# Kernel tuning notes

Measured on AMD Instinct MI355X. Metric: run time of the kernel, lower is better.

Reference implementation:

```python
import jax, jax.numpy as jnp
import numpy as np

N_NODES = 50000
N_EDGES = 800000
G_DIM = 128
H1_DIM = 128
H2_DIM = 128
N_REL = 8          # 2 * n_speakers**2, n_speakers = 2
N_BASES = 30


def setup_inputs() -> dict:
    key = jax.random.key(0)
    ks = jax.random.split(key, 10)
    node_features = jax.random.normal(ks[0], (N_NODES, G_DIM), jnp.float32)
    edge_index = jax.random.randint(ks[1], (2, N_EDGES), 0, N_NODES, jnp.int32)
    edge_norm = jax.random.uniform(ks[2], (N_EDGES,), jnp.float32)
    edge_type = jax.random.randint(ks[3], (N_EDGES,), 0, N_REL, jnp.int32)
    # RGCN basis-decomposition params
    w_comp = jax.random.normal(ks[4], (N_REL, N_BASES), jnp.float32) / np.sqrt(N_BASES)
    bases = jax.random.normal(ks[5], (N_BASES, G_DIM, H1_DIM), jnp.float32) / np.sqrt(G_DIM)
    loop_weight = jax.random.normal(ks[6], (G_DIM, H1_DIM), jnp.float32) / np.sqrt(G_DIM)
    bias1 = jnp.zeros((H1_DIM,), jnp.float32)
    # GraphConv params
    W2 = jax.random.normal(ks[7], (H1_DIM, H2_DIM), jnp.float32) / np.sqrt(H1_DIM)
    bias2 = jnp.zeros((H2_DIM,), jnp.float32)
    return dict(node_features=node_features, edge_index=edge_index,
                edge_norm=edge_norm, edge_type=edge_type,
                w_comp=w_comp, bases=bases, loop_weight=loop_weight, bias1=bias1,
                W2=W2, bias2=bias2)


def reference(node_features, edge_index, edge_norm, edge_type,
              w_comp, bases, loop_weight, bias1, W2, bias2):
    N = node_features.shape[0]
    src, dst = edge_index[0], edge_index[1]

    # ---- RGCNConv (DGL RelGraphConv, basis regularizer, self_loop + bias) ----
    # relation weights from bases: [R, g, h1]
    weight = jnp.einsum('rb,bio->rio', w_comp, bases)
    # project all nodes by every relation (R is small), then gather per edge
    xw = jnp.einsum('ni,rio->rno', node_features, weight)   # [R, N, h1]
    msgs = xw[edge_type, src] * edge_norm[:, None]          # [E, h1]
    agg = jax.ops.segment_sum(msgs, dst, num_segments=N)    # scatter-add to dst
    h = agg + node_features @ loop_weight + bias1           # [N, h1]

    # ---- GraphConv (DGL, norm='both', edge_weight; degrees are UNweighted) ----
    ones = jnp.ones_like(edge_norm)
    out_deg = jax.ops.segment_sum(ones, src, num_segments=N)
    in_deg = jax.ops.segment_sum(ones, dst, num_segments=N)
    norm_src = jnp.clip(out_deg, 1.0) ** -0.5               # [N]
    norm_dst = jnp.clip(in_deg, 1.0) ** -0.5                # [N]
    m2 = (h * norm_src[:, None])[src] * edge_norm[:, None]  # [E, h1]
    agg2 = jax.ops.segment_sum(m2, dst, num_segments=N)     # [N, h1]
    out = (agg2 * norm_dst[:, None]) @ W2 + bias2           # [N, h2]
    return out
```

## Files before the change

kernel.cpp:

```cpp
#include <hip/hip_runtime.h>

#define NN 50000
#define EE 800000
#define NB 30
#define NJ 1152
#define NSB 49
#define NPART 16
#define RANGE 3136
#define NSLICE 64
#define ESL 12500
#define NPAD 50176

typedef __attribute__((ext_vector_type(8))) short short8;
typedef __attribute__((ext_vector_type(4))) float f32x4;

__device__ __forceinline__ unsigned short f2bf(float f) {
  unsigned u = __float_as_uint(f);
  u += 0x7FFF + ((u >> 16) & 1);
  return (unsigned short)(u >> 16);
}
__device__ __forceinline__ float bf2f(unsigned short s) {
  return __uint_as_float(((unsigned)s) << 16);
}

__global__ __launch_bounds__(256) void k_prep(const float* __restrict__ wcomp,
                                              const float* __restrict__ bases,
                                              const float* __restrict__ loopw,
                                              const float* __restrict__ W2,
                                              const float* __restrict__ X,
                                              unsigned short* __restrict__ Wt,
                                              unsigned short* __restrict__ W2t,
                                              unsigned short* __restrict__ Xbf) {
  int b = blockIdx.x;
  if (b < 576) {
    int idx = b * 256 + threadIdx.x;
    int j = idx >> 7, k = idx & 127;
    float v;
    if (j < 1024) {
      int r = j >> 7, o = j & 127;
      float s = 0.f;
#pragma unroll
      for (int bb = 0; bb < NB; ++bb)
        s = fmaf(wcomp[r * NB + bb], bases[((size_t)bb * 128 + k) * 128 + o], s);
      v = s;
    } else {
      v = loopw[k * 128 + (j - 1024)];
    }
    Wt[idx] = f2bf(v);
    if (idx < 128 * 128) W2t[idx] = f2bf(W2[k * 128 + j]);
  } else {
    int i = ((b - 576) * 256 + threadIdx.x) * 4;
    float4 v = *(const float4*)(X + i);
    uint2 o;
    o.x = (unsigned)f2bf(v.x) | ((unsigned)f2bf(v.y) << 16);
    o.y = (unsigned)f2bf(v.z) | ((unsigned)f2bf(v.w) << 16);
    *(uint2*)(Xbf + i) = o;
  }
}

__global__ __launch_bounds__(256) void k_hist(const int* __restrict__ EI,
                                              int* __restrict__ pdin, int* __restrict__ pdout) {
  __shared__ int hist[RANGE];
  int b = blockIdx.x;
  int kind = b & 1;
  int sl = (b >> 1) & (NSLICE - 1);
  int r = b >> 7;
  const int base = r * RANGE;
  const int* vals = kind ? EI : EI + EE;
  int* part = kind ? pdout : pdin;
  for (int j = threadIdx.x; j < RANGE; j += 256) hist[j] = 0;
  __syncthreads();
  const int e0 = sl * ESL;
  for (int i = threadIdx.x; i < ESL / 4; i += 256) {
    int4 d = *(const int4*)(vals + e0 + i * 4);
    int x;
    x = d.x - base; if ((unsigned)x < RANGE) atomicAdd(&hist[x], 1);
    x = d.y - base; if ((unsigned)x < RANGE) atomicAdd(&hist[x], 1);
    x = d.z - base; if ((unsigned)x < RANGE) atomicAdd(&hist[x], 1);
    x = d.w - base; if ((unsigned)x < RANGE) atomicAdd(&hist[x], 1);
  }
  __syncthreads();
  for (int j = threadIdx.x; j < RANGE; j += 256)
    part[sl * NPAD + base + j] = hist[j];
}

__global__ __launch_bounds__(256) void k_scan_a(const int* __restrict__ pdin,
                                                const int* __restrict__ pdout,
                                                int* __restrict__ din,
                                                int* __restrict__ dout,
                                                int* __restrict__ bsum) {
  __shared__ int wsum[4];
  int b = blockIdx.x, t = threadIdx.x;
  int lane = t & 63, w = t >> 6;
  int i0 = b * 1024 + t * 4;
  int4 acc = {0, 0, 0, 0}, od = {0, 0, 0, 0};
  for (int sl = 0; sl < NSLICE; ++sl) {
    int4 a = *(const int4*)(pdin + sl * NPAD + i0);
    int4 o = *(const int4*)(pdout + sl * NPAD + i0);
    acc.x += a.x; acc.y += a.y; acc.z += a.z; acc.w += a.w;
    od.x += o.x; od.y += o.y; od.z += o.z; od.w += o.w;
  }
  *(int4*)(din + i0) = acc;
  *(int4*)(dout + i0) = od;
  int sv = acc.x + acc.y + acc.z + acc.w;
#pragma unroll
  for (int off = 32; off; off >>= 1) sv += __shfl_down(sv, off, 64);
  if (lane == 0) wsum[w] = sv;
  __syncthreads();
  if (t == 0) bsum[b] = wsum[0] + wsum[1] + wsum[2] + wsum[3];
}

__global__ void k_scan_b(int* __restrict__ bsum, int* __restrict__ row_ptr) {
  int t = threadIdx.x;
  int v = (t < NSB) ? bsum[t] : 0;
  int orig = v;
#pragma unroll
  for (int off = 1; off < 64; off <<= 1) {
    int u = __shfl_up(v, off, 64);
    if (t >= off) v += u;
  }
  if (t < NSB) bsum[t] = v - orig;
  if (t == 0) row_ptr[NN] = EE;
}

__global__ __launch_bounds__(256) void k_scan_c(const int* __restrict__ din,
                                                const int* __restrict__ bsum,
                                                int* __restrict__ row_ptr,
                                                int* __restrict__ cursor) {
  __shared__ int wsum[4];
  int b = blockIdx.x, t = threadIdx.x;
  int lane = t & 63, w = t >> 6;
  int i0 = b * 1024 + t * 4;
  int4 d = *(const int4*)(din + i0);
  int sth = d.x + d.y + d.z + d.w;
  int v = sth;
#pragma unroll
  for (int off = 1; off < 64; off <<= 1) {
    int u = __shfl_up(v, off, 64);
    if (lane >= off) v += u;
  }
  if (lane == 63) wsum[w] = v;
  __syncthreads();
  int woff = 0;
  for (int j = 0; j < w; ++j) woff += wsum[j];
  int base = bsum[b] + woff + (v - sth);
  if (i0 + 0 <= NN) { row_ptr[i0 + 0] = base; if (i0 + 0 < NN) cursor[i0 + 0] = base; } base += d.x;
  if (i0 + 1 <= NN) { row_ptr[i0 + 1] = base; if (i0 + 1 < NN) cursor[i0 + 1] = base; } base += d.y;
  if (i0 + 2 <= NN) { row_ptr[i0 + 2] = base; if (i0 + 2 < NN) cursor[i0 + 2] = base; } base += d.z;
  if (i0 + 3 <= NN) { row_ptr[i0 + 3] = base; if (i0 + 3 < NN) cursor[i0 + 3] = base; }
}

__global__ void k_csr(const int* __restrict__ src, const int* __restrict__ dst,
                      const int* __restrict__ ety, const float* __restrict__ enorm,
                      int* __restrict__ cursor, int2* __restrict__ em1) {
  int e = blockIdx.x * 256 + threadIdx.x;
  if (e < EE) {
    int pos = atomicAdd(&cursor[dst[e]], 1);
    int s = src[e];
    int wb = __float_as_int(enorm[e]);
    em1[pos] = make_int2(s * NJ + ety[e] * 128, wb);
  }
}

__global__ __launch_bounds__(256) void k_gemm(const unsigned short* __restrict__ A,
                                              const unsigned short* __restrict__ B,
                                              unsigned short* __restrict__ Cbf,
                                              float* __restrict__ Cf,
                                              const float* __restrict__ bias,
                                              int M, int ldc) {
  __shared__ unsigned short As[128 * 136];
  __shared__ unsigned short Bs[128 * 136];
  const int m0 = blockIdx.x * 128, j0 = blockIdx.y * 128;
  const int t = threadIdx.x;
  for (int i = t; i < 2048; i += 256) {
    int r = i >> 4, c = i & 15;
    uint4 va = {0, 0, 0, 0};
    int gr = m0 + r;
    if (gr < M) va = *(const uint4*)(A + (size_t)gr * 128 + c * 8);
    *(uint4*)(&As[r * 136 + c * 8]) = va;
    uint4 vb = *(const uint4*)(B + (size_t)(j0 + r) * 128 + c * 8);
    *(uint4*)(&Bs[r * 136 + c * 8]) = vb;
  }
  __syncthreads();

  const int lane = t & 63, wave = t >> 6;
  const int wr = (wave >> 1) * 64, wc = (wave & 1) * 64;
  const int lr = lane & 15, lk = (lane >> 4) * 8;

  f32x4 acc[4][4];
#pragma unroll
  for (int m = 0; m < 4; ++m)
#pragma unroll
    for (int n = 0; n < 4; ++n) acc[m][n] = (f32x4){0.f, 0.f, 0.f, 0.f};

#pragma unroll
  for (int kt = 0; kt < 4; ++kt) {
    short8 af[4], bfr[4];
#pragma unroll
    for (int m = 0; m < 4; ++m)
      af[m] = *(const short8*)(&As[(wr + m * 16 + lr) * 136 + kt * 32 + lk]);
#pragma unroll
    for (int n = 0; n < 4; ++n)
      bfr[n] = *(const short8*)(&Bs[(wc + n * 16 + lr) * 136 + kt * 32 + lk]);
#pragma unroll
    for (int m = 0; m < 4; ++m)
#pragma unroll
      for (int n = 0; n < 4; ++n)
        acc[m][n] = __builtin_amdgcn_mfma_f32_16x16x32_bf16(af[m], bfr[n], acc[m][n], 0, 0, 0);
  }

#pragma unroll
  for (int m = 0; m < 4; ++m) {
    int rbase = m0 + wr + m * 16 + (lane >> 4) * 4;
#pragma unroll
    for (int i = 0; i < 4; ++i) {
      int row = rbase + i;
      if (row >= M) continue;
      if (Cbf) {
        unsigned short* cr = Cbf + (size_t)row * ldc + j0 + wc;
#pragma unroll
        for (int n = 0; n < 4; ++n) cr[n * 16 + lr] = f2bf(acc[m][n][i]);
      } else {
        float* cr = Cf + (size_t)row * ldc + j0 + wc;
#pragma unroll
        for (int n = 0; n < 4; ++n) cr[n * 16 + lr] = acc[m][n][i] + bias[j0 + wc + n * 16 + lr];
      }
    }
  }
}

#define UNR 8

__global__ __launch_bounds__(256) void k_agg1(const unsigned short* __restrict__ xw,
                                              const int2* __restrict__ em1,
                                              const int* __restrict__ row_ptr,
                                              const int* __restrict__ deg_out,
                                              const float* __restrict__ bias1,
                                              unsigned short* __restrict__ hs) {
  int gw = (blockIdx.x * blockDim.x + threadIdx.x) >> 6;
  int lane = threadIdx.x & 63;
  if (gw >= NN) return;
  int beg = row_ptr[gw], end = row_ptr[gw + 1];
  float a0 = 0.f, a1 = 0.f;
  for (int i = beg; i < end; i += UNR) {
    int2 md[UNR];
    unsigned v[UNR];
#pragma unroll
    for (int j = 0; j < UNR; ++j) {
      int idx = i + j;
      idx = idx < end ? idx : end - 1;
      md[j] = em1[idx];
      if (i + j >= end) md[j].y = 0;
    }
#pragma unroll
    for (int j = 0; j < UNR; ++j)
      v[j] = *(const unsigned*)(xw + (size_t)(unsigned)md[j].x + lane * 2);
#pragma unroll
    for (int j = 0; j < UNR; ++j) {
      float w = __int_as_float(md[j].y);
      a0 = fmaf(w, bf2f((unsigned short)(v[j] & 0xffff)), a0);
      a1 = fmaf(w, bf2f((unsigned short)(v[j] >> 16)), a1);
    }
  }
  unsigned vl = *(const unsigned*)(xw + (size_t)gw * NJ + 1024 + lane * 2);
  float ns = rsqrtf(fmaxf((float)deg_out[gw], 1.f));
  float h0 = (a0 + bf2f((unsigned short)(vl & 0xffff)) + bias1[lane * 2]) * ns;
  float h1 = (a1 + bf2f((unsigned short)(vl >> 16)) + bias1[lane * 2 + 1]) * ns;
  unsigned o = (unsigned)f2bf(h0) | ((unsigned)f2bf(h1) << 16);
  *(unsigned*)(hs + (size_t)gw * 128 + lane * 2) = o;
}

__global__ __launch_bounds__(256) void k_agg2(const unsigned short* __restrict__ hs,
                                              const int2* __restrict__ em1,
                                              const int* __restrict__ row_ptr,
                                              unsigned short* __restrict__ zb) {
  int gw = (blockIdx.x * blockDim.x + threadIdx.x) >> 6;
  int lane = threadIdx.x & 63;
  if (gw >= NN) return;
  int beg = row_ptr[gw], end = row_ptr[gw + 1];
  float a0 = 0.f, a1 = 0.f;
  for (int i = beg; i < end; i += UNR) {
    int2 md[UNR];
    unsigned v[UNR];
#pragma unroll
    for (int j = 0; j < UNR; ++j) {
      int idx = i + j;
      idx = idx < end ? idx : end - 1;
      md[j] = em1[idx];
      if (i + j >= end) md[j].y = 0;
    }
#pragma unroll
    for (int j = 0; j < UNR; ++j) {
      unsigned srcn = (((unsigned)md[j].x) >> 7) / 9u;
      v[j] = *(const unsigned*)(hs + ((size_t)srcn << 7) + lane * 2);
    }
#pragma unroll
    for (int j = 0; j < UNR; ++j) {
      float w = __int_as_float(md[j].y);
      a0 = fmaf(w, bf2f((unsigned short)(v[j] & 0xffff)), a0);
      a1 = fmaf(w, bf2f((unsigned short)(v[j] >> 16)), a1);
    }
  }
  float nd = rsqrtf(fmaxf((float)(end - beg), 1.f));
  unsigned o = (unsigned)f2bf(a0 * nd) | ((unsigned)f2bf(a1 * nd) << 16);
  *(unsigned*)(zb + (size_t)gw * 128 + lane * 2) = o;
}

extern "C" void kernel_launch(void* const* d_in, const int* in_sizes, int n_in,
                              void* d_out, int out_size, void* d_ws, size_t ws_size,
                              hipStream_t stream) {
  const float* X = (const float*)d_in[0];
  const int* EI = (const int*)d_in[1];
  const float* enorm = (const float*)d_in[2];
  const int* etype = (const int*)d_in[3];
  const float* wcomp = (const float*)d_in[4];
  const float* bases = (const float*)d_in[5];
  const float* loopw = (const float*)d_in[6];
  const float* bias1 = (const float*)d_in[7];
  const float* W2 = (const float*)d_in[8];
  const float* bias2 = (const float*)d_in[9];
  float* out = (float*)d_out;
  const int* srcA = EI;
  const int* dstA = EI + EE;

  char* p = (char*)d_ws;
  auto alloc = [&](size_t bytes) {
    char* r = p;
    p += (bytes + 255) & ~(size_t)255;
    return r;
  };
  unsigned short* xw  = (unsigned short*)alloc((size_t)NN * NJ * 2);
  unsigned short* Xbf = (unsigned short*)alloc((size_t)NN * 128 * 2);
  unsigned short* hs  = (unsigned short*)alloc((size_t)NN * 128 * 2);
  unsigned short* zb  = (unsigned short*)alloc((size_t)NN * 128 * 2);
  unsigned short* Wt  = (unsigned short*)alloc((size_t)NJ * 128 * 2);
  unsigned short* W2t = (unsigned short*)alloc(128 * 128 * 2);
  int* pdin    = (int*)alloc((size_t)NSLICE * NPAD * 4);
  int* pdout   = (int*)alloc((size_t)NSLICE * NPAD * 4);
  int* din     = (int*)alloc((size_t)NPAD * 4);
  int* dout    = (int*)alloc((size_t)NPAD * 4);
  int* row_ptr = (int*)alloc((size_t)(NPAD + 1) * 4);
  int* cursor  = (int*)alloc((size_t)NN * 4);
  int* bsum    = (int*)alloc((size_t)NSB * 4);
  int2* em1    = (int2*)alloc((size_t)EE * 8);

  hipLaunchKernelGGL(k_prep, dim3(6826), dim3(256), 0, stream,
                     wcomp, bases, loopw, W2, X, Wt, W2t, Xbf);
  hipLaunchKernelGGL(k_hist, dim3(2048), dim3(256), 0, stream, EI, pdin, pdout);
  hipLaunchKernelGGL(k_scan_a, dim3(NSB), dim3(256), 0, stream, pdin, pdout, din, dout, bsum);
  hipLaunchKernelGGL(k_scan_b, dim3(1), dim3(64), 0, stream, bsum, row_ptr);
  hipLaunchKernelGGL(k_scan_c, dim3(NSB), dim3(256), 0, stream, din, bsum, row_ptr, cursor);
  hipLaunchKernelGGL(k_csr, dim3(3125), dim3(256), 0, stream,
                     srcA, dstA, etype, enorm, cursor, em1);
  hipLaunchKernelGGL(k_gemm, dim3(391, 9), dim3(256), 0, stream,
                     Xbf, Wt, xw, (float*)nullptr, (const float*)nullptr, NN, NJ);
  hipLaunchKernelGGL(k_agg1, dim3(12500), dim3(256), 0, stream,
                     xw, em1, row_ptr, dout, bias1, hs);
  hipLaunchKernelGGL(k_agg2, dim3(12500), dim3(256), 0, stream,
                     hs, em1, row_ptr, zb);
  hipLaunchKernelGGL(k_gemm, dim3(391, 1), dim3(256), 0, stream,
                     zb, W2t, (unsigned short*)nullptr, out, bias2, NN, 128);
}
```

Measured before the change: 330.0 us.

## Replace global-atomic CSR fill with per-slice prefix offsets and LDS-atomic scatter

Removes the per-edge global atomicAdd on a cursor array when building the dst-sorted edge list. It converts the existing per-slice in-degree histogram into per-slice starting offsets, then each block handles one edge slice and one node range, placing edges with shared-memory atomics. This avoids contended global atomics but makes every block scan its whole slice's dst array (16 node ranges each read every slice), adding redundant reads and one more kernel launch.

Result: no change. 325.3 us (-1.4%).

```diff
diff --git a/kernel.cpp b/kernel.cpp
--- a/kernel.cpp
+++ b/kernel.cpp
@@ -125,8 +125,7 @@
 
 __global__ __launch_bounds__(256) void k_scan_c(const int* __restrict__ din,
                                                 const int* __restrict__ bsum,
-                                                int* __restrict__ row_ptr,
-                                                int* __restrict__ cursor) {
+                                                int* __restrict__ row_ptr) {
   __shared__ int wsum[4];
   int b = blockIdx.x, t = threadIdx.x;
   int lane = t & 63, w = t >> 6;
@@ -144,21 +143,52 @@
   int woff = 0;
   for (int j = 0; j < w; ++j) woff += wsum[j];
   int base = bsum[b] + woff + (v - sth);
-  if (i0 + 0 <= NN) { row_ptr[i0 + 0] = base; if (i0 + 0 < NN) cursor[i0 + 0] = base; } base += d.x;
-  if (i0 + 1 <= NN) { row_ptr[i0 + 1] = base; if (i0 + 1 < NN) cursor[i0 + 1] = base; } base += d.y;
-  if (i0 + 2 <= NN) { row_ptr[i0 + 2] = base; if (i0 + 2 < NN) cursor[i0 + 2] = base; } base += d.z;
-  if (i0 + 3 <= NN) { row_ptr[i0 + 3] = base; if (i0 + 3 < NN) cursor[i0 + 3] = base; }
-}
-
-__global__ void k_csr(const int* __restrict__ src, const int* __restrict__ dst,
-                      const int* __restrict__ ety, const float* __restrict__ enorm,
-                      int* __restrict__ cursor, int2* __restrict__ em1) {
-  int e = blockIdx.x * 256 + threadIdx.x;
-  if (e < EE) {
-    int pos = atomicAdd(&cursor[dst[e]], 1);
-    int s = src[e];
-    int wb = __float_as_int(enorm[e]);
-    em1[pos] = make_int2(s * NJ + ety[e] * 128, wb);
+  if (i0 + 0 <= NN) row_ptr[i0 + 0] = base; base += d.x;
+  if (i0 + 1 <= NN) row_ptr[i0 + 1] = base; base += d.y;
+  if (i0 + 2 <= NN) row_ptr[i0 + 2] = base; base += d.z;
+  if (i0 + 3 <= NN) row_ptr[i0 + 3] = base;
+}
+
+__global__ __launch_bounds__(256) void k_pfx(int* __restrict__ pdin,
+                                             const int* __restrict__ row_ptr) {
+  int n = blockIdx.x * 256 + threadIdx.x;
+  int run = row_ptr[n];
+#pragma unroll 8
+  for (int sl = 0; sl < NSLICE; ++sl) {
+    int c = pdin[sl * NPAD + n];
+    pdin[sl * NPAD + n] = run;
+    run += c;
+  }
+}
+
+__global__ __launch_bounds__(256) void k_scatter(const int* __restrict__ src,
+                                                 const int* __restrict__ dst,
+                                                 const int* __restrict__ ety,
+                                                 const float* __restrict__ enorm,
+                                                 const int* __restrict__ pdin,
+                                                 int2* __restrict__ em1) {
+  __shared__ int cur[RANGE];
+  int b = blockIdx.x;
+  int sl = b & (NSLICE - 1), r = b >> 6;
+  const int base = r * RANGE;
+  for (int j = threadIdx.x; j < RANGE; j += 256)
+    cur[j] = pdin[sl * NPAD + base + j];
+  __syncthreads();
+  const int e0 = sl * ESL;
+  for (int i = threadIdx.x; i < ESL / 4; i += 256) {
+    int4 d = *(const int4*)(dst + e0 + i * 4);
+    int vals[4] = {d.x, d.y, d.z, d.w};
+#pragma unroll
+    for (int j = 0; j < 4; ++j) {
+      int dv = vals[j] - base;
+      if ((unsigned)dv < RANGE) {
+        int e = e0 + i * 4 + j;
+        int pos = atomicAdd(&cur[dv], 1);
+        int sv = src[e];
+        int wb = __float_as_int(enorm[e]);
+        em1[pos] = make_int2(sv * NJ + ety[e] * 128, wb);
+      }
+    }
   }
 }
 
@@ -340,7 +370,6 @@
   int* din     = (int*)alloc((size_t)NPAD * 4);
   int* dout    = (int*)alloc((size_t)NPAD * 4);
   int* row_ptr = (int*)alloc((size_t)(NPAD + 1) * 4);
-  int* cursor  = (int*)alloc((size_t)NN * 4);
   int* bsum    = (int*)alloc((size_t)NSB * 4);
   int2* em1    = (int2*)alloc((size_t)EE * 8);
 
@@ -349,9 +378,10 @@
   hipLaunchKernelGGL(k_hist, dim3(2048), dim3(256), 0, stream, EI, pdin, pdout);
   hipLaunchKernelGGL(k_scan_a, dim3(NSB), dim3(256), 0, stream, pdin, pdout, din, dout, bsum);
   hipLaunchKernelGGL(k_scan_b, dim3(1), dim3(64), 0, stream, bsum, row_ptr);
-  hipLaunchKernelGGL(k_scan_c, dim3(NSB), dim3(256), 0, stream, din, bsum, row_ptr, cursor);
-  hipLaunchKernelGGL(k_csr, dim3(3125), dim3(256), 0, stream,
-                     srcA, dstA, etype, enorm, cursor, em1);
+  hipLaunchKernelGGL(k_scan_c, dim3(NSB), dim3(256), 0, stream, din, bsum, row_ptr);
+  hipLaunchKernelGGL(k_pfx, dim3(NPAD / 256), dim3(256), 0, stream, pdin, row_ptr);
+  hipLaunchKernelGGL(k_scatter, dim3(1024), dim3(256), 0, stream,
+                     srcA, dstA, etype, enorm, pdin, em1);
   hipLaunchKernelGGL(k_gemm, dim3(391, 9), dim3(256), 0, stream,
                      Xbf, Wt, xw, (float*)nullptr, (const float*)nullptr, NN, NJ);
   hipLaunchKernelGGL(k_agg1, dim3(12500), dim3(256), 0, stream,
```
